# Kernel tuning notes

Hardware: AMD Instinct MI355X
Metric: run time of the kernel (lower is better)

Reference implementation:

```python
import jax, jax.numpy as jnp
import numpy as np

N_NODES = 50000
N_EDGES = 800000
IN_CH = 256
HID = 512
NUM_LAYERS = 3
EPS = 1e-12  # F.normalize eps


def setup_inputs() -> dict:
    key = jax.random.key(0)
    ks = jax.random.split(key, 2 + 3 * NUM_LAYERS)
    x = jax.random.normal(ks[0], (N_NODES, IN_CH), dtype=jnp.float32)
    edge_index = jax.random.randint(ks[1], (2, N_EDGES), 0, N_NODES, dtype=jnp.int64)
    inp = {"x": x, "edge_index": edge_index}
    dims = [(IN_CH, HID)] + [(HID, HID)] * (NUM_LAYERS - 1)
    for i, (din, dout) in enumerate(dims):
        s = 1.0 / np.sqrt(din)
        inp[f"Wl{i}"] = jax.random.normal(ks[2 + 3 * i], (din, dout), dtype=jnp.float32) * s
        inp[f"bl{i}"] = jnp.zeros((dout,), dtype=jnp.float32)
        inp[f"Wr{i}"] = jax.random.normal(ks[3 + 3 * i], (din, dout), dtype=jnp.float32) * s
    return inp


def _sage_conv(x, src, dst, Wl, bl, Wr):
    # aggr='add': out[dst] += x[src], then lin_l(agg) + lin_r(x), L2 normalize rows
    agg = jax.ops.segment_sum(x[src], dst, num_segments=x.shape[0])  # [N, din]
    out = agg @ Wl + bl + x @ Wr  # [N, dout]
    norm = jnp.maximum(jnp.linalg.norm(out, axis=-1, keepdims=True), EPS)
    return out / norm


def reference(x, edge_index, Wl0, bl0, Wr0, Wl1, bl1, Wr1, Wl2, bl2, Wr2):
    src, dst = edge_index[0], edge_index[1]
    feat = x
    params = [(Wl0, bl0, Wr0), (Wl1, bl1, Wr1), (Wl2, bl2, Wr2)]
    for Wl, bl, Wr in params:
        aggre = _sage_conv(feat, src, dst, Wl, bl, Wr)
        # Dropout(p=0.15) is identity in eval mode
        feat = jax.nn.elu(aggre)
    return feat
```

## Files before the change

### kernel.cpp

```cpp
#include <hip/hip_runtime.h>
#include <math.h>

#define N_NODES 50000
#define M_PAD   50048
#define N_EDGES 800000
#define HID 512

typedef short bf16x8 __attribute__((ext_vector_type(8)));
typedef float f32x4  __attribute__((ext_vector_type(4)));
typedef unsigned short u16x4 __attribute__((ext_vector_type(4)));

__device__ inline float b2f(unsigned short u) {
    union { unsigned int i; float f; } v; v.i = ((unsigned int)u) << 16; return v.f;
}
__device__ inline unsigned short f2b(float f) {
    union { float f; unsigned int i; } v; v.f = f;
    unsigned int r = v.i + 0x7FFFu + ((v.i >> 16) & 1u);
    return (unsigned short)(r >> 16);
}


__global__ void zero_kernel(int* __restrict__ p, int n) {
    int i = blockIdx.x * blockDim.x + threadIdx.x;
    if (i < n) p[i] = 0;
}

__global__ void detect_kernel(const int* __restrict__ e, int* __restrict__ flag) {
    if (blockIdx.x == 0 && threadIdx.x == 0) {
        int is64 = 1;
        for (int i = 0; i < 16; ++i)
            if (e[2 * i + 1] != 0) is64 = 0;
        *flag = is64;
    }
}

__global__ void hist_kernel(const void* __restrict__ eidx, const int* __restrict__ flag,
                            int* __restrict__ counts) {
    int e = blockIdx.x * blockDim.x + threadIdx.x;
    if (e >= N_EDGES) return;
    int is64 = *flag;
    int d;
    if (is64) d = (int)((const long long*)eidx)[N_EDGES + e];
    else      d = ((const int*)eidx)[N_EDGES + e];
    atomicAdd(&counts[d], 1);
}

__global__ __launch_bounds__(1024) void scan_kernel(const int* __restrict__ counts,
                                                    int* __restrict__ offsets) {
    __shared__ int sums[1024];
    int t = threadIdx.x;
    const int CH = (N_NODES + 1023) / 1024;
    int lo = t * CH;
    int hi = min(lo + CH, N_NODES);
    int s = 0;
    for (int i = lo; i < hi; ++i) s += counts[i];
    sums[t] = s;
    __syncthreads();
    for (int off = 1; off < 1024; off <<= 1) {
        int v = 0;
        if (t >= off) v = sums[t - off];
        __syncthreads();
        sums[t] += v;
        __syncthreads();
    }
    int excl = (t == 0) ? 0 : sums[t - 1];
    for (int i = lo; i < hi; ++i) { offsets[i] = excl; excl += counts[i]; }
    if (t == 1023) offsets[N_NODES] = excl;
}

__global__ void fill_kernel(const void* __restrict__ eidx, const int* __restrict__ flag,
                            const int* __restrict__ offsets, int* __restrict__ cursor,
                            int* __restrict__ edge_src) {
    int e = blockIdx.x * blockDim.x + threadIdx.x;
    if (e >= N_EDGES) return;
    int is64 = *flag;
    int s, d;
    if (is64) {
        const long long* p = (const long long*)eidx;
        s = (int)p[e];
        d = (int)p[N_EDGES + e];
    } else {
        const int* p = (const int*)eidx;
        s = p[e];
        d = p[N_EDGES + e];
    }
    int pos = atomicAdd(&cursor[d], 1);
    edge_src[offsets[d] + pos] = s;
}


__global__ __launch_bounds__(256) void xconv_kernel(const float* __restrict__ x,
                                                    unsigned short* __restrict__ Fh) {
    int id = blockIdx.x * 256 + threadIdx.x;
    if (id >= M_PAD * 64) return;
    int row = id >> 6;
    int c = (id & 63) * 4;
    float4 v = make_float4(0.f, 0.f, 0.f, 0.f);
    if (row < N_NODES) v = *(const float4*)(x + (size_t)row * 256 + c);
    ushort4 h;
    h.x = f2b(v.x); h.y = f2b(v.y); h.z = f2b(v.z); h.w = f2b(v.w);
    *(ushort4*)(Fh + (size_t)row * 256 + c) = h;
}

__global__ __launch_bounds__(128) void wconv_kernel(const float* __restrict__ W,
                                                    unsigned short* __restrict__ T, int K) {
    int n = blockIdx.x;
    for (int k = threadIdx.x; k < K; k += 128)
        T[(size_t)n * K + k] = f2b(W[(size_t)k * HID + n]);
}


template <int EPL>
__global__ __launch_bounds__(256) void aggregate_kernel(const unsigned short* __restrict__ Fh,
                                                        const int* __restrict__ off,
                                                        const int* __restrict__ esrc,
                                                        unsigned short* __restrict__ Ah) {
    const int W = EPL * 64;
    const int wid = threadIdx.x >> 6;
    const int lane = threadIdx.x & 63;
    const int node = blockIdx.x * 4 + wid;
    if (node >= N_NODES) return;
    const int beg = off[node], end = off[node + 1];
    const int deg = end - beg;

    float a0[EPL], a1[EPL];
#pragma unroll
    for (int j = 0; j < EPL; ++j) { a0[j] = 0.f; a1[j] = 0.f; }

    int idxv = (beg + lane < end) ? esrc[beg + lane] : 0;
    for (int i = 0; i < deg; i += 2) {
        const int b = i & 63;
        if (b == 0 && i)
            idxv = (beg + i + lane < end) ? esrc[beg + i + lane] : 0;
        {
            const int s = __shfl(idxv, b);
            const unsigned short* r = Fh + (size_t)s * W + lane * EPL;
#pragma unroll
            for (int q = 0; q < EPL / 4; ++q) {
                u16x4 v = *(const u16x4*)(r + q * 4);
#pragma unroll
                for (int j = 0; j < 4; ++j) a0[q * 4 + j] += b2f(v[j]);
            }
        }
        if (i + 1 < deg) {
            const int s = __shfl(idxv, b + 1);
            const unsigned short* r = Fh + (size_t)s * W + lane * EPL;
#pragma unroll
            for (int q = 0; q < EPL / 4; ++q) {
                u16x4 v = *(const u16x4*)(r + q * 4);
#pragma unroll
                for (int j = 0; j < 4; ++j) a1[q * 4 + j] += b2f(v[j]);
            }
        }
    }

    unsigned short* op = Ah + (size_t)node * W + lane * EPL;
#pragma unroll
    for (int q = 0; q < EPL / 4; ++q) {
        u16x4 h;
#pragma unroll
        for (int j = 0; j < 4; ++j) h[j] = f2b(a0[q * 4 + j] + a1[q * 4 + j]);
        *(u16x4*)(op + q * 4) = h;
    }
}


__global__ __launch_bounds__(256) void gemm_mfma_kernel(
    const unsigned short* __restrict__ A, const unsigned short* __restrict__ F,
    const unsigned short* __restrict__ W1, const unsigned short* __restrict__ W2,
    const float* __restrict__ bias, float* __restrict__ out, int Ks) {
    __shared__ unsigned short S[2 * 16384];
    const int bm = blockIdx.y * 128;
    const int bn = blockIdx.x * 128;
    const int tid = threadIdx.x;
    const int l = tid & 63;
    const int w = tid >> 6;
    const int wr = (w >> 1) * 64;
    const int wc = (w & 1) * 64;
    const int arow = l >> 2;
    const int acol = (l & 3) * 8;

    const unsigned short* wsrc = (w == 0) ? A : (w == 1) ? F : (w == 2) ? W1 : W2;
    const int rb = (w < 2) ? bm : bn;
    const unsigned short* gbase = wsrc + (size_t)(rb + arow) * Ks + acol;
    const size_t cstride = (size_t)16 * Ks;

    f32x4 acc[4][4];
#pragma unroll
    for (int m = 0; m < 4; ++m)
#pragma unroll
        for (int n = 0; n < 4; ++n) acc[m][n] = (f32x4){0.f, 0.f, 0.f, 0.f};

    const int aoff = (wr + (l & 15)) * 32 + (l >> 4) * 8;
    const int woff = (wc + (l & 15)) * 32 + (l >> 4) * 8;
    const int ktiles = Ks >> 5;

    auto STAGE = [&](int buf, int kt) {
        const unsigned short* g = gbase + kt * 32;
        unsigned short* lb = &S[buf * 16384 + w * 4096];
#pragma unroll
        for (int c = 0; c < 8; ++c) {
            __builtin_amdgcn_global_load_lds(
                (const __attribute__((address_space(1))) void*)(g + (size_t)c * cstride),
                (__attribute__((address_space(3))) void*)(lb + c * 512), 16, 0, 0);
        }
    };

    STAGE(0, 0);
    __syncthreads();

    for (int kt = 0; kt < ktiles; ++kt) {
        if (kt + 1 < ktiles) STAGE((kt + 1) & 1, kt + 1);
        const int sb = (kt & 1) * 16384;

        bf16x8 af[4], ff[4], w1f[4], w2f[4];
#pragma unroll
        for (int m = 0; m < 4; ++m) {
            af[m] = *(const bf16x8*)&S[sb + aoff + m * 512];
            ff[m] = *(const bf16x8*)&S[sb + 4096 + aoff + m * 512];
        }
#pragma unroll
        for (int n = 0; n < 4; ++n) {
            w1f[n] = *(const bf16x8*)&S[sb + 8192 + woff + n * 512];
            w2f[n] = *(const bf16x8*)&S[sb + 12288 + woff + n * 512];
        }
#pragma unroll
        for (int m = 0; m < 4; ++m)
#pragma unroll
            for (int n = 0; n < 4; ++n) {
                acc[m][n] = __builtin_amdgcn_mfma_f32_16x16x32_bf16(af[m], w1f[n], acc[m][n], 0, 0, 0);
                acc[m][n] = __builtin_amdgcn_mfma_f32_16x16x32_bf16(ff[m], w2f[n], acc[m][n], 0, 0, 0);
            }
        __syncthreads();
    }

    const int r0 = bm + wr + (l >> 4) * 4;
    const int c0 = bn + wc + (l & 15);
#pragma unroll
    for (int n = 0; n < 4; ++n) {
        const float bv = bias[c0 + n * 16];
#pragma unroll
        for (int m = 0; m < 4; ++m) {
#pragma unroll
            for (int j = 0; j < 4; ++j) {
                int gr = r0 + m * 16 + j;
                if (gr < N_NODES)
                    out[(size_t)gr * HID + c0 + n * 16] = acc[m][n][j] + bv;
            }
        }
    }
}


template <int FINAL>
__global__ __launch_bounds__(256) void norm_elu_kernel(const float* __restrict__ in,
                                                       float* __restrict__ outF,
                                                       unsigned short* __restrict__ Fh) {
    const int wid = threadIdx.x >> 6;
    const int lane = threadIdx.x & 63;
    const int row = blockIdx.x * 4 + wid;
    if (row >= N_NODES) return;
    const float* p = in + (size_t)row * HID + lane * 8;
    float4 v0 = *(const float4*)p;
    float4 v1 = *(const float4*)(p + 4);
    float ss = v0.x * v0.x + v0.y * v0.y + v0.z * v0.z + v0.w * v0.w
             + v1.x * v1.x + v1.y * v1.y + v1.z * v1.z + v1.w * v1.w;
#pragma unroll
    for (int o = 32; o > 0; o >>= 1) ss += __shfl_xor(ss, o);
    float inv = 1.f / fmaxf(sqrtf(ss), 1e-12f);
    float r[8] = {v0.x, v0.y, v0.z, v0.w, v1.x, v1.y, v1.z, v1.w};
#pragma unroll
    for (int j = 0; j < 8; ++j) {
        r[j] *= inv;
        r[j] = r[j] > 0.f ? r[j] : expm1f(r[j]);
    }
    if (FINAL) {
        float* q = outF + (size_t)row * HID + lane * 8;
        *(float4*)q = make_float4(r[0], r[1], r[2], r[3]);
        *(float4*)(q + 4) = make_float4(r[4], r[5], r[6], r[7]);
    } else {
        unsigned short* q = Fh + (size_t)row * HID + lane * 8;
        u16x4 h0, h1;
#pragma unroll
        for (int j = 0; j < 4; ++j) { h0[j] = f2b(r[j]); h1[j] = f2b(r[4 + j]); }
        *(u16x4*)q = h0;
        *(u16x4*)(q + 4) = h1;
    }
}


extern "C" void kernel_launch(void* const* d_in, const int* in_sizes, int n_in,
                              void* d_out, int out_size, void* d_ws, size_t ws_size,
                              hipStream_t stream) {
    const float* x    = (const float*)d_in[0];
    const void*  eidx = d_in[1];
    const float* Wl0 = (const float*)d_in[2];
    const float* bl0 = (const float*)d_in[3];
    const float* Wr0 = (const float*)d_in[4];
    const float* Wl1 = (const float*)d_in[5];
    const float* bl1 = (const float*)d_in[6];
    const float* Wr1 = (const float*)d_in[7];
    const float* Wl2 = (const float*)d_in[8];
    const float* bl2 = (const float*)d_in[9];
    const float* Wr2 = (const float*)d_in[10];
    float* outF = (float*)d_out;

    char* ws = (char*)d_ws;
    size_t o = 0;
    auto alloc = [&](size_t bytes) { void* p = ws + o; o += (bytes + 255) & ~(size_t)255; return p; };

    const size_t PLANE = (size_t)M_PAD * 512 * 2;
    unsigned short* FhB = (unsigned short*)alloc(PLANE);
    unsigned short* AhB = (unsigned short*)alloc(PLANE);

    unsigned short* Wl0t = (unsigned short*)alloc(512 * 256 * 2);
    unsigned short* Wr0t = (unsigned short*)alloc(512 * 256 * 2);
    unsigned short* Wl1t = (unsigned short*)alloc(512 * 512 * 2);
    unsigned short* Wr1t = (unsigned short*)alloc(512 * 512 * 2);
    unsigned short* Wl2t = (unsigned short*)alloc(512 * 512 * 2);
    unsigned short* Wr2t = (unsigned short*)alloc(512 * 512 * 2);

    int* counts   = (int*)alloc((size_t)2 * N_NODES * 4);
    int* cursor   = counts + N_NODES;
    int* offsets  = (int*)alloc((size_t)(N_NODES + 1) * 4);
    int* edge_src = (int*)alloc((size_t)N_EDGES * 4);
    int* flag     = (int*)alloc(256);

    zero_kernel<<<(2 * N_NODES + 255) / 256, 256, 0, stream>>>(counts, 2 * N_NODES);
    detect_kernel<<<1, 64, 0, stream>>>((const int*)eidx, flag);
    hist_kernel<<<(N_EDGES + 255) / 256, 256, 0, stream>>>(eidx, flag, counts);
    scan_kernel<<<1, 1024, 0, stream>>>(counts, offsets);
    fill_kernel<<<(N_EDGES + 255) / 256, 256, 0, stream>>>(eidx, flag, offsets, cursor, edge_src);

    xconv_kernel<<<(M_PAD * 64 + 255) / 256, 256, 0, stream>>>(x, FhB);
    wconv_kernel<<<512, 128, 0, stream>>>(Wl0, Wl0t, 256);
    wconv_kernel<<<512, 128, 0, stream>>>(Wr0, Wr0t, 256);
    wconv_kernel<<<512, 128, 0, stream>>>(Wl1, Wl1t, 512);
    wconv_kernel<<<512, 128, 0, stream>>>(Wr1, Wr1t, 512);
    wconv_kernel<<<512, 128, 0, stream>>>(Wl2, Wl2t, 512);
    wconv_kernel<<<512, 128, 0, stream>>>(Wr2, Wr2t, 512);

    dim3 ggrid(4, M_PAD / 128);
    const int ngrid = (N_NODES + 3) / 4;

    aggregate_kernel<4><<<ngrid, 256, 0, stream>>>(FhB, offsets, edge_src, AhB);
    gemm_mfma_kernel<<<ggrid, 256, 0, stream>>>(AhB, FhB, Wl0t, Wr0t, bl0, outF, 256);
    norm_elu_kernel<0><<<ngrid, 256, 0, stream>>>(outF, nullptr, FhB);

    aggregate_kernel<8><<<ngrid, 256, 0, stream>>>(FhB, offsets, edge_src, AhB);
    gemm_mfma_kernel<<<ggrid, 256, 0, stream>>>(AhB, FhB, Wl1t, Wr1t, bl1, outF, 512);
    norm_elu_kernel<0><<<ngrid, 256, 0, stream>>>(outF, nullptr, FhB);

    aggregate_kernel<8><<<ngrid, 256, 0, stream>>>(FhB, offsets, edge_src, AhB);
    gemm_mfma_kernel<<<ggrid, 256, 0, stream>>>(AhB, FhB, Wl2t, Wr2t, bl2, outF, 512);
    norm_elu_kernel<1><<<ngrid, 256, 0, stream>>>(outF, outF, nullptr);

    (void)in_sizes; (void)n_in; (void)out_size; (void)ws_size;
}
```

Measured before the change: 862.5 us.

## Concatenate aggregated and self features into one K-doubled GEMM operand

Stores aggregated features and node features side by side in a single row-interleaved buffer, and stores Wl and Wr concatenated along K. The dual-operand GEMM becomes a single GEMM with twice the K, which halves the LDS tile (16 KB double-buffered), lets every wave stage both A and B, and adds a launch-bounds occupancy hint. In exchange, the aggregate gathers now read rows with doubled stride, which spreads the gathered data over more memory and may lower cache efficiency.

```diff
diff --git a/kernel.cpp b/kernel.cpp
--- a/kernel.cpp
+++ b/kernel.cpp
@@ -90,7 +90,7 @@
 
 
 __global__ __launch_bounds__(256) void xconv_kernel(const float* __restrict__ x,
-                                                    unsigned short* __restrict__ Fh) {
+                                                    unsigned short* __restrict__ cat1) {
     int id = blockIdx.x * 256 + threadIdx.x;
     if (id >= M_PAD * 64) return;
     int row = id >> 6;
@@ -99,14 +99,15 @@
     if (row < N_NODES) v = *(const float4*)(x + (size_t)row * 256 + c);
     ushort4 h;
     h.x = f2b(v.x); h.y = f2b(v.y); h.z = f2b(v.z); h.w = f2b(v.w);
-    *(ushort4*)(Fh + (size_t)row * 256 + c) = h;
+    *(ushort4*)(cat1 + (size_t)row * 512 + 256 + c) = h;
 }
 
 __global__ __launch_bounds__(128) void wconv_kernel(const float* __restrict__ W,
-                                                    unsigned short* __restrict__ T, int K) {
+                                                    unsigned short* __restrict__ T,
+                                                    int K, int ktot, int off) {
     int n = blockIdx.x;
     for (int k = threadIdx.x; k < K; k += 128)
-        T[(size_t)n * K + k] = f2b(W[(size_t)k * HID + n]);
+        T[(size_t)n * ktot + off + k] = f2b(W[(size_t)k * HID + n]);
 }
 
 
@@ -116,6 +117,7 @@
                                                         const int* __restrict__ esrc,
                                                         unsigned short* __restrict__ Ah) {
     const int W = EPL * 64;
+    const int STRIDE = 2 * W;
     const int wid = threadIdx.x >> 6;
     const int lane = threadIdx.x & 63;
     const int node = blockIdx.x * 4 + wid;
@@ -134,7 +136,7 @@
             idxv = (beg + i + lane < end) ? esrc[beg + i + lane] : 0;
         {
             const int s = __shfl(idxv, b);
-            const unsigned short* r = Fh + (size_t)s * W + lane * EPL;
+            const unsigned short* r = Fh + (size_t)s * STRIDE + lane * EPL;
 #pragma unroll
             for (int q = 0; q < EPL / 4; ++q) {
                 u16x4 v = *(const u16x4*)(r + q * 4);
@@ -144,7 +146,7 @@
         }
         if (i + 1 < deg) {
             const int s = __shfl(idxv, b + 1);
-            const unsigned short* r = Fh + (size_t)s * W + lane * EPL;
+            const unsigned short* r = Fh + (size_t)s * STRIDE + lane * EPL;
 #pragma unroll
             for (int q = 0; q < EPL / 4; ++q) {
                 u16x4 v = *(const u16x4*)(r + q * 4);
@@ -154,7 +156,7 @@
         }
     }
 
-    unsigned short* op = Ah + (size_t)node * W + lane * EPL;
+    unsigned short* op = Ah + (size_t)node * STRIDE + lane * EPL;
 #pragma unroll
     for (int q = 0; q < EPL / 4; ++q) {
         u16x4 h;
@@ -165,11 +167,10 @@
 }
 
 
-__global__ __launch_bounds__(256) void gemm_mfma_kernel(
-    const unsigned short* __restrict__ A, const unsigned short* __restrict__ F,
-    const unsigned short* __restrict__ W1, const unsigned short* __restrict__ W2,
-    const float* __restrict__ bias, float* __restrict__ out, int Ks) {
-    __shared__ unsigned short S[2 * 16384];
+__global__ __launch_bounds__(256, 4) void gemm_mfma_kernel(
+    const unsigned short* __restrict__ A, const unsigned short* __restrict__ B,
+    const float* __restrict__ bias, float* __restrict__ out, int K) {
+    __shared__ unsigned short S[2 * 8192];
     const int bm = blockIdx.y * 128;
     const int bn = blockIdx.x * 128;
     const int tid = threadIdx.x;
@@ -180,10 +181,8 @@
     const int arow = l >> 2;
     const int acol = (l & 3) * 8;
 
-    const unsigned short* wsrc = (w == 0) ? A : (w == 1) ? F : (w == 2) ? W1 : W2;
-    const int rb = (w < 2) ? bm : bn;
-    const unsigned short* gbase = wsrc + (size_t)(rb + arow) * Ks + acol;
-    const size_t cstride = (size_t)16 * Ks;
+    const unsigned short* gA = A + (size_t)(bm + arow) * K + acol;
+    const unsigned short* gB = B + (size_t)(bn + arow) * K + acol;
 
     f32x4 acc[4][4];
 #pragma unroll
@@ -193,16 +192,19 @@
 
     const int aoff = (wr + (l & 15)) * 32 + (l >> 4) * 8;
     const int woff = (wc + (l & 15)) * 32 + (l >> 4) * 8;
-    const int ktiles = Ks >> 5;
+    const int ktiles = K >> 5;
 
     auto STAGE = [&](int buf, int kt) {
-        const unsigned short* g = gbase + kt * 32;
-        unsigned short* lb = &S[buf * 16384 + w * 4096];
-#pragma unroll
-        for (int c = 0; c < 8; ++c) {
+        unsigned short* lb = &S[buf * 8192];
+#pragma unroll
+        for (int i = 0; i < 2; ++i) {
+            const int c = w * 2 + i;
             __builtin_amdgcn_global_load_lds(
-                (const __attribute__((address_space(1))) void*)(g + (size_t)c * cstride),
+                (const __attribute__((address_space(1))) void*)(gA + (size_t)(c * 16) * K + kt * 32),
                 (__attribute__((address_space(3))) void*)(lb + c * 512), 16, 0, 0);
+            __builtin_amdgcn_global_load_lds(
+                (const __attribute__((address_space(1))) void*)(gB + (size_t)(c * 16) * K + kt * 32),
+                (__attribute__((address_space(3))) void*)(lb + 4096 + c * 512), 16, 0, 0);
         }
     };
 
@@ -211,26 +213,20 @@
 
     for (int kt = 0; kt < ktiles; ++kt) {
         if (kt + 1 < ktiles) STAGE((kt + 1) & 1, kt + 1);
-        const int sb = (kt & 1) * 16384;
-
-        bf16x8 af[4], ff[4], w1f[4], w2f[4];
-#pragma unroll
-        for (int m = 0; m < 4; ++m) {
+        const int sb = (kt & 1) * 8192;
+
+        bf16x8 af[4], wf[4];
+#pragma unroll
+        for (int m = 0; m < 4; ++m)
             af[m] = *(const bf16x8*)&S[sb + aoff + m * 512];
-            ff[m] = *(const bf16x8*)&S[sb + 4096 + aoff + m * 512];
-        }
-#pragma unroll
-        for (int n = 0; n < 4; ++n) {
-            w1f[n] = *(const bf16x8*)&S[sb + 8192 + woff + n * 512];
-            w2f[n] = *(const bf16x8*)&S[sb + 12288 + woff + n * 512];
-        }
+#pragma unroll
+        for (int n = 0; n < 4; ++n)
+            wf[n] = *(const bf16x8*)&S[sb + 4096 + woff + n * 512];
 #pragma unroll
         for (int m = 0; m < 4; ++m)
 #pragma unroll
-            for (int n = 0; n < 4; ++n) {
-                acc[m][n] = __builtin_amdgcn_mfma_f32_16x16x32_bf16(af[m], w1f[n], acc[m][n], 0, 0, 0);
-                acc[m][n] = __builtin_amdgcn_mfma_f32_16x16x32_bf16(ff[m], w2f[n], acc[m][n], 0, 0, 0);
-            }
+            for (int n = 0; n < 4; ++n)
+                acc[m][n] = __builtin_amdgcn_mfma_f32_16x16x32_bf16(af[m], wf[n], acc[m][n], 0, 0, 0);
         __syncthreads();
     }
 
@@ -279,7 +275,7 @@
         *(float4*)q = make_float4(r[0], r[1], r[2], r[3]);
         *(float4*)(q + 4) = make_float4(r[4], r[5], r[6], r[7]);
     } else {
-        unsigned short* q = Fh + (size_t)row * HID + lane * 8;
+        unsigned short* q = Fh + (size_t)row * 1024 + lane * 8;
         u16x4 h0, h1;
 #pragma unroll
         for (int j = 0; j < 4; ++j) { h0[j] = f2b(r[j]); h1[j] = f2b(r[4 + j]); }
@@ -309,16 +305,12 @@
     size_t o = 0;
     auto alloc = [&](size_t bytes) { void* p = ws + o; o += (bytes + 255) & ~(size_t)255; return p; };
 
-    const size_t PLANE = (size_t)M_PAD * 512 * 2;
-    unsigned short* FhB = (unsigned short*)alloc(PLANE);
-    unsigned short* AhB = (unsigned short*)alloc(PLANE);
-
-    unsigned short* Wl0t = (unsigned short*)alloc(512 * 256 * 2);
-    unsigned short* Wr0t = (unsigned short*)alloc(512 * 256 * 2);
-    unsigned short* Wl1t = (unsigned short*)alloc(512 * 512 * 2);
-    unsigned short* Wr1t = (unsigned short*)alloc(512 * 512 * 2);
-    unsigned short* Wl2t = (unsigned short*)alloc(512 * 512 * 2);
-    unsigned short* Wr2t = (unsigned short*)alloc(512 * 512 * 2);
+    unsigned short* Cat1 = (unsigned short*)alloc((size_t)M_PAD * 512 * 2);
+    unsigned short* Cat2 = (unsigned short*)alloc((size_t)M_PAD * 1024 * 2);
+
+    unsigned short* Wcat0 = (unsigned short*)alloc(512 * 512 * 2);
+    unsigned short* Wcat1 = (unsigned short*)alloc(512 * 1024 * 2);
+    unsigned short* Wcat2 = (unsigned short*)alloc(512 * 1024 * 2);
 
     int* counts   = (int*)alloc((size_t)2 * N_NODES * 4);
     int* cursor   = counts + N_NODES;
@@ -332,27 +324,27 @@
     scan_kernel<<<1, 1024, 0, stream>>>(counts, offsets);
     fill_kernel<<<(N_EDGES + 255) / 256, 256, 0, stream>>>(eidx, flag, offsets, cursor, edge_src);
 
-    xconv_kernel<<<(M_PAD * 64 + 255) / 256, 256, 0, stream>>>(x, FhB);
-    wconv_kernel<<<512, 128, 0, stream>>>(Wl0, Wl0t, 256);
-    wconv_kernel<<<512, 128, 0, stream>>>(Wr0, Wr0t, 256);
-    wconv_kernel<<<512, 128, 0, stream>>>(Wl1, Wl1t, 512);
-    wconv_kernel<<<512, 128, 0, stream>>>(Wr1, Wr1t, 512);
-    wconv_kernel<<<512, 128, 0, stream>>>(Wl2, Wl2t, 512);
-    wconv_kernel<<<512, 128, 0, stream>>>(Wr2, Wr2t, 512);
+    xconv_kernel<<<(M_PAD * 64 + 255) / 256, 256, 0, stream>>>(x, Cat1);
+    wconv_kernel<<<512, 128, 0, stream>>>(Wl0, Wcat0, 256, 512, 0);
+    wconv_kernel<<<512, 128, 0, stream>>>(Wr0, Wcat0, 256, 512, 256);
+    wconv_kernel<<<512, 128, 0, stream>>>(Wl1, Wcat1, 512, 1024, 0);
+    wconv_kernel<<<512, 128, 0, stream>>>(Wr1, Wcat1, 512, 1024, 512);
+    wconv_kernel<<<512, 128, 0, stream>>>(Wl2, Wcat2, 512, 1024, 0);
+    wconv_kernel<<<512, 128, 0, stream>>>(Wr2, Wcat2, 512, 1024, 512);
 
     dim3 ggrid(4, M_PAD / 128);
     const int ngrid = (N_NODES + 3) / 4;
 
-    aggregate_kernel<4><<<ngrid, 256, 0, stream>>>(FhB, offsets, edge_src, AhB);
-    gemm_mfma_kernel<<<ggrid, 256, 0, stream>>>(AhB, FhB, Wl0t, Wr0t, bl0, outF, 256);
-    norm_elu_kernel<0><<<ngrid, 256, 0, stream>>>(outF, nullptr, FhB);
-
-    aggregate_kernel<8><<<ngrid, 256, 0, stream>>>(FhB, offsets, edge_src, AhB);
-    gemm_mfma_kernel<<<ggrid, 256, 0, stream>>>(AhB, FhB, Wl1t, Wr1t, bl1, outF, 512);
-    norm_elu_kernel<0><<<ngrid, 256, 0, stream>>>(outF, nullptr, FhB);
-
-    aggregate_kernel<8><<<ngrid, 256, 0, stream>>>(FhB, offsets, edge_src, AhB);
-    gemm_mfma_kernel<<<ggrid, 256, 0, stream>>>(AhB, FhB, Wl2t, Wr2t, bl2, outF, 512);
+    aggregate_kernel<4><<<ngrid, 256, 0, stream>>>(Cat1 + 256, offsets, edge_src, Cat1);
+    gemm_mfma_kernel<<<ggrid, 256, 0, stream>>>(Cat1, Wcat0, bl0, outF, 512);
+    norm_elu_kernel<0><<<ngrid, 256, 0, stream>>>(outF, nullptr, Cat2 + 512);
+
+    aggregate_kernel<8><<<ngrid, 256, 0, stream>>>(Cat2 + 512, offsets, edge_src, Cat2);
+    gemm_mfma_kernel<<<ggrid, 256, 0, stream>>>(Cat2, Wcat1, bl1, outF, 1024);
+    norm_elu_kernel<0><<<ngrid, 256, 0, stream>>>(outF, nullptr, Cat2 + 512);
+
+    aggregate_kernel<8><<<ngrid, 256, 0, stream>>>(Cat2 + 512, offsets, edge_src, Cat2);
+    gemm_mfma_kernel<<<ggrid, 256, 0, stream>>>(Cat2, Wcat2, bl2, outF, 1024);
     norm_elu_kernel<1><<<ngrid, 256, 0, stream>>>(outF, outF, nullptr);
 
     (void)in_sizes; (void)n_in; (void)out_size; (void)ws_size;
```

New measurement: 809.3 us. -6.2%, faster.
